# Performance work log

Measured on AMD Instinct MI355X. Metric: run time of the kernel, lower is better.

The kernel has to match this reference:

```python
import jax, jax.numpy as jnp
import numpy as np

WH, WW = 7, 7
DIM, HEADS = 256, 8


def make_table_index(wh, ww):
    # relative coords table (log-spaced CPB input) and relative position index
    ch = np.arange(-(wh - 1), wh, dtype=np.float32)
    cw = np.arange(-(ww - 1), ww, dtype=np.float32)
    t = np.stack(np.meshgrid(ch, cw, indexing='ij'), axis=-1)[None]  # [1,2wh-1,2ww-1,2]
    t = t.copy()
    t[..., 0] /= (wh - 1)
    t[..., 1] /= (ww - 1)
    t *= 8.0
    t = np.sign(t) * np.log2(np.abs(t) + 1.0) / np.log2(8.0)
    coords = np.stack(np.meshgrid(np.arange(wh), np.arange(ww), indexing='ij'))
    cf = coords.reshape(2, -1)
    rc = (cf[:, :, None] - cf[:, None, :]).transpose(1, 2, 0).copy()  # [N,N,2]
    rc[..., 0] += wh - 1
    rc[..., 1] += ww - 1
    rc[..., 0] *= 2 * ww - 1
    idx = rc.sum(-1)
    return t.astype(np.float32), idx.astype(np.int32)


def setup_inputs() -> dict:
    key = jax.random.key(0)
    ks = jax.random.split(key, 10)
    B_, N, C, H = 2048, WH * WW, DIM, HEADS
    table, idx = make_table_index(WH, WW)
    return {
        'x': jax.random.normal(ks[0], (B_, N, C), jnp.float32),
        'mask': jnp.zeros((64, N, N), jnp.float32),
        'qkv_w': jax.random.normal(ks[1], (3 * C, C), jnp.float32) * 0.02,
        'q_bias': jnp.zeros((C,), jnp.float32),
        'v_bias': jnp.zeros((C,), jnp.float32),
        'logit_scale': jnp.full((H, 1, 1), np.log(10.0), jnp.float32),
        'cpb_w1': jax.random.normal(ks[2], (512, 2), jnp.float32) * 0.02,
        'cpb_b1': jnp.zeros((512,), jnp.float32),
        'cpb_w2': jax.random.normal(ks[3], (H, 512), jnp.float32) * 0.02,
        'proj_w': jax.random.normal(ks[4], (C, C), jnp.float32) * 0.02,
        'proj_b': jnp.zeros((C,), jnp.float32),
        'rel_coords_table': jnp.asarray(table),
        'rel_pos_index': jnp.asarray(idx),
    }


def _l2norm(t):
    return t / jnp.maximum(jnp.linalg.norm(t, axis=-1, keepdims=True), 1e-12)


def reference(x, mask, qkv_w, q_bias, v_bias, logit_scale, cpb_w1, cpb_b1,
              cpb_w2, proj_w, proj_b, rel_coords_table, rel_pos_index):
    B_, N, C = x.shape
    H = logit_scale.shape[0]
    hd = C // H
    qkv_b = jnp.concatenate([q_bias, jnp.zeros_like(v_bias), v_bias])
    qkv = (x @ qkv_w.T + qkv_b).reshape(B_, N, 3, H, hd).transpose(2, 0, 3, 1, 4)
    q, k, v = qkv[0], qkv[1], qkv[2]  # [B_,H,N,hd]
    attn = jnp.einsum('bhnd,bhmd->bhnm', _l2norm(q), _l2norm(k))
    scale = jnp.exp(jnp.minimum(logit_scale, jnp.log(jnp.float32(100.0))))  # [H,1,1]
    attn = attn * scale[None]
    # CPB MLP -> relative position bias
    table = jax.nn.relu(rel_coords_table @ cpb_w1.T + cpb_b1) @ cpb_w2.T  # [1,Th,Tw,H]
    table = table.reshape(-1, H)
    bias = table[rel_pos_index.reshape(-1)].reshape(N, N, H).transpose(2, 0, 1)
    attn = attn + 16.0 * jax.nn.sigmoid(bias)[None]
    nW = mask.shape[0]
    attn = attn.reshape(B_ // nW, nW, H, N, N) + mask[None, :, None]
    attn = jax.nn.softmax(attn.reshape(B_, H, N, N), axis=-1)
    out = jnp.einsum('bhnm,bhmd->bhnd', attn, v).transpose(0, 2, 1, 3).reshape(B_, N, C)
    return out @ proj_w.T + proj_b
```

## Files before the change

### kernel.cpp

```cpp
#include <hip/hip_runtime.h>

#define DEV __device__ __forceinline__

typedef float  f32x4  __attribute__((ext_vector_type(4)));
typedef __bf16 bf16x4 __attribute__((ext_vector_type(4)));
typedef __bf16 bf16x8 __attribute__((ext_vector_type(8)));

DEV unsigned short f2bf(float f) {
  unsigned u = __float_as_uint(f);
  u += 0x7fffu + ((u >> 16) & 1u);
  return (unsigned short)(u >> 16);
}

DEV void cp16(const void* g, void* l) {
  __builtin_amdgcn_global_load_lds((const __attribute__((address_space(1))) void*)g,
                                   (__attribute__((address_space(3))) void*)l, 16, 0, 0);
}

__global__ __launch_bounds__(256) void prep_kernel(
    const float* __restrict__ qkv_w, const float* __restrict__ proj_w,
    const float* __restrict__ q_bias, const float* __restrict__ v_bias,
    unsigned short* __restrict__ wq, unsigned short* __restrict__ wp,
    float* __restrict__ qkvb)
{
  int gid = blockIdx.x * 256 + threadIdx.x;
  if (gid < 196608) wq[gid] = f2bf(qkv_w[gid]);
  else              wp[gid - 196608] = f2bf(proj_w[gid - 196608]);
  if (gid < 768)
    qkvb[gid] = (gid < 256) ? q_bias[gid] : ((gid < 512) ? 0.f : v_bias[gid - 512]);
}

__global__ __launch_bounds__(256) void xbf16(
    const float* __restrict__ X, unsigned short* __restrict__ Xb)
{
  size_t gid = (size_t)blockIdx.x * 256 + threadIdx.x;
  const float4* xp = (const float4*)X;
  float4 f0 = xp[2 * gid], f1 = xp[2 * gid + 1];
  bf16x8 u;
  u[0] = (__bf16)f0.x; u[1] = (__bf16)f0.y; u[2] = (__bf16)f0.z; u[3] = (__bf16)f0.w;
  u[4] = (__bf16)f1.x; u[5] = (__bf16)f1.y; u[6] = (__bf16)f1.z; u[7] = (__bf16)f1.w;
  ((bf16x8*)Xb)[gid] = u;
}

__global__ __launch_bounds__(64) void cpb_mlp(
    const float* __restrict__ tab, const float* __restrict__ w1,
    const float* __restrict__ b1, const float* __restrict__ w2,
    float* __restrict__ table16)
{
  int r = blockIdx.x;
  int t = threadIdx.x;
  float x0 = tab[r * 2 + 0], x1 = tab[r * 2 + 1];
  float part[8];
#pragma unroll
  for (int h = 0; h < 8; ++h) part[h] = 0.f;
  for (int j = t; j < 512; j += 64) {
    float hv = fmaxf(w1[j * 2 + 0] * x0 + w1[j * 2 + 1] * x1 + b1[j], 0.f);
#pragma unroll
    for (int h = 0; h < 8; ++h) part[h] += hv * w2[h * 512 + j];
  }
#pragma unroll
  for (int h = 0; h < 8; ++h) {
    float v = part[h];
    for (int off = 32; off > 0; off >>= 1) v += __shfl_down(v, off, 64);
    if (t == 0) table16[r * 8 + h] = 16.f / (1.f + expf(-v));
  }
}

__global__ __launch_bounds__(256) void bmb(
    const float* __restrict__ t16, const int* __restrict__ ridx,
    const float* __restrict__ mask, float* __restrict__ bias64,
    float* __restrict__ mask64)
{
  const float L2E = 1.44269504f;
  int gid = blockIdx.x * 256 + threadIdx.x;
  int p = gid & 4095, i = p >> 6, j = p & 63;
  bool valid = (i < 49) && (j < 49);
  if (gid < 32768) {
    int h = gid >> 12;
    bias64[gid] = valid ? t16[ridx[i * 49 + j] * 8 + h] * L2E : -1e30f;
  } else {
    int g2 = gid - 32768;
    int w = g2 >> 12;
    mask64[g2] = valid ? mask[w * 2401 + i * 49 + j] * L2E : 0.f;
  }
}

__global__ __launch_bounds__(256) void qkv_attn(
    const unsigned short* __restrict__ Xb, const unsigned short* __restrict__ W,
    const float* __restrict__ qkvb, const float* __restrict__ logit_scale,
    const float* __restrict__ bias64, const float* __restrict__ mask64,
    unsigned short* __restrict__ aout)
{
  __shared__ __align__(1024) char smem[65536];
  const int t = threadIdx.x, w = t >> 6, l = t & 63, quad = l >> 4, l15 = l & 15;
  char* sX  = smem;
  char* myr = smem + 32768 + w * 8192;

  const int win = blockIdx.x;
  const int wtok = win * 49;

  {
    const int r0 = w * 16;
    const int s = l & 31;
#pragma unroll
    for (int i = 0; i < 8; ++i) {
      const int row = r0 + 2 * i + (l >> 5);
      if (row < 49) {
        const unsigned short* src = Xb + (size_t)(wtok + row) * 256
                                  + (s >> 3) * 64 + (((s & 7) ^ (row & 7)) * 8);
        cp16(src, sX + (r0 + 2 * i) * 512);
      } else {
        uint4 z; z.x = z.y = z.z = z.w = 0u;
        *(uint4*)(sX + row * 512 + s * 16) = z;
      }
    }
  }
  __syncthreads();

  const int bslot = (quad ^ ((l15 >> 1) & 3)) * 16;

  auto do_gemm = [&](int wrb, f32x4 (&acc)[2][4]) {
#pragma unroll
    for (int kt = 0; kt < 4; ++kt)
#pragma unroll
      for (int kk = 0; kk < 2; ++kk) {
        bf16x8 wf[2], xf[4];
#pragma unroll
        for (int nt = 0; nt < 2; ++nt)
          wf[nt] = *(const bf16x8*)(W + (size_t)(wrb + nt * 16 + l15) * 256
                                      + kt * 64 + (4 * kk + quad) * 8);
#pragma unroll
        for (int mA = 0; mA < 4; ++mA)
          xf[mA] = *(const bf16x8*)(sX + (mA * 16 + l15) * 512 + kt * 128
                                       + (((4 * kk + quad) ^ (l15 & 7)) * 16));
#pragma unroll
        for (int nt = 0; nt < 2; ++nt)
#pragma unroll
          for (int mA = 0; mA < 4; ++mA)
            acc[nt][mA] = __builtin_amdgcn_mfma_f32_16x16x32_bf16(wf[nt], xf[mA], acc[nt][mA], 0, 0, 0);
      }
  };

  auto bounce = [&](f32x4 (&acc)[2][4], const float* bias, bf16x8 (&f)[4]) {
    const f32x4 b0 = *(const f32x4*)(bias + quad * 4);
    const f32x4 b1 = *(const f32x4*)(bias + 16 + quad * 4);
#pragma unroll
    for (int mA = 0; mA < 4; ++mA) {
      bf16x8 u;
      u[0] = (__bf16)(acc[0][mA][0] + b0[0]); u[1] = (__bf16)(acc[0][mA][1] + b0[1]);
      u[2] = (__bf16)(acc[0][mA][2] + b0[2]); u[3] = (__bf16)(acc[0][mA][3] + b0[3]);
      u[4] = (__bf16)(acc[1][mA][0] + b1[0]); u[5] = (__bf16)(acc[1][mA][1] + b1[1]);
      u[6] = (__bf16)(acc[1][mA][2] + b1[2]); u[7] = (__bf16)(acc[1][mA][3] + b1[3]);
      *(bf16x8*)(myr + (mA * 16 + l15) * 64 + bslot) = u;
    }
    asm volatile("s_waitcnt lgkmcnt(0)" ::: "memory");
    __builtin_amdgcn_sched_barrier(0);
#pragma unroll
    for (int mt = 0; mt < 4; ++mt)
      f[mt] = *(const bf16x8*)(myr + (mt * 16 + l15) * 64 + bslot);
  };

#pragma unroll 1
  for (int hh = 0; hh < 2; ++hh) {
    const int h = 2 * w + hh;

    f32x4 ka[2][4] = {};
    do_gemm(256 + h * 32, ka);
    bf16x8 kf[4];
    bounce(ka, qkvb + 256 + h * 32, kf);

    f32x4 qa[2][4] = {};
    do_gemm(h * 32, qa);
    bf16x8 qf[4];
    bounce(qa, qkvb + h * 32, qf);

    const float scale = __expf(fminf(logit_scale[h], 4.60517019f)) * 1.44269504f;
    float rqv[4];
#pragma unroll
    for (int nt = 0; nt < 4; ++nt) {
      float s = 0.f;
#pragma unroll
      for (int d = 0; d < 8; ++d) { float f = (float)qf[nt][d]; s += f * f; }
      s += __shfl_xor(s, 16, 64); s += __shfl_xor(s, 32, 64);
      rqv[nt] = scale / fmaxf(sqrtf(s), 1e-12f);
    }
    float rkl[4];
#pragma unroll
    for (int mt = 0; mt < 4; ++mt) {
      float s = 0.f;
#pragma unroll
      for (int d = 0; d < 8; ++d) { float f = (float)kf[mt][d]; s += f * f; }
      s += __shfl_xor(s, 16, 64); s += __shfl_xor(s, 32, 64);
      rkl[mt] = 1.f / fmaxf(sqrtf(s), 1e-12f);
    }
    f32x4 rk4v[4];
#pragma unroll
    for (int mt = 0; mt < 4; ++mt)
#pragma unroll
      for (int r = 0; r < 4; ++r)
        rk4v[mt][r] = __shfl(rkl[mt], (quad << 2) + r, 16);

    {
      f32x4 va[2][4] = {};
      do_gemm(512 + h * 32, va);
      const f32x4 vb0 = *(const f32x4*)(qkvb + 512 + h * 32 + quad * 4);
      const f32x4 vb1 = *(const f32x4*)(qkvb + 512 + h * 32 + 16 + quad * 4);
#pragma unroll
      for (int mA = 0; mA < 4; ++mA) {
        const int tok = mA * 16 + l15;
#pragma unroll
        for (int nt = 0; nt < 2; ++nt) {
#pragma unroll
          for (int r = 0; r < 4; ++r) {
            const int d = nt * 16 + quad * 4 + r;
            *(__bf16*)(myr + d * 128 + (((tok >> 3) ^ (d & 7)) << 4) + (tok & 7) * 2) =
                (__bf16)(va[nt][mA][r] + (nt ? vb1[r] : vb0[r]));
          }
        }
      }
    }
    asm volatile("s_waitcnt lgkmcnt(0)" ::: "memory");
    __builtin_amdgcn_sched_barrier(0);
    bf16x8 vf[2][2];
#pragma unroll
    for (int kk = 0; kk < 2; ++kk)
#pragma unroll
      for (int mt = 0; mt < 2; ++mt)
        vf[kk][mt] = *(const bf16x8*)(myr + (mt * 16 + l15) * 128
                                          + (((4 * kk + quad) ^ (l15 & 7)) * 16));
    asm volatile("s_waitcnt lgkmcnt(0)" ::: "memory");
    __builtin_amdgcn_sched_barrier(0);

    f32x4 sacc[4][4] = {};
    __builtin_amdgcn_s_setprio(1);
#pragma unroll
    for (int mt = 0; mt < 4; ++mt)
#pragma unroll
      for (int nt = 0; nt < 4; ++nt)
        sacc[mt][nt] = __builtin_amdgcn_mfma_f32_16x16x32_bf16(kf[mt], qf[nt], sacc[mt][nt], 0, 0, 0);
    __builtin_amdgcn_s_setprio(0);

    unsigned short* P = (unsigned short*)myr;
    const float* bh = bias64 + (size_t)h * 4096;
    const float* mw = mask64 + (size_t)(win & 63) * 4096;
    float rs4[4];
#pragma unroll
    for (int nt = 0; nt < 4; ++nt) {
      const int i = nt * 16 + l15;
      const float rqi = rqv[nt];
      float mx = -3e38f;
#pragma unroll
      for (int mt = 0; mt < 4; ++mt) {
        const int jb = mt * 16 + quad * 4;
        const f32x4 b4 = *(const f32x4*)(bh + i * 64 + jb);
        const f32x4 m4 = *(const f32x4*)(mw + i * 64 + jb);
#pragma unroll
        for (int r = 0; r < 4; ++r) {
          float sv = fmaf(sacc[mt][nt][r], rqi * rk4v[mt][r], b4[r] + m4[r]);
          sacc[mt][nt][r] = sv;
          mx = fmaxf(mx, sv);
        }
      }
      mx = fmaxf(mx, __shfl_xor(mx, 16, 64));
      mx = fmaxf(mx, __shfl_xor(mx, 32, 64));
      float sum = 0.f;
#pragma unroll
      for (int mt = 0; mt < 4; ++mt) {
        float pv[4];
#pragma unroll
        for (int r = 0; r < 4; ++r) {
          pv[r] = __builtin_amdgcn_exp2f(sacc[mt][nt][r] - mx);
          sum += pv[r];
        }
        bf16x4 pk;
        pk[0] = (__bf16)pv[0]; pk[1] = (__bf16)pv[1];
        pk[2] = (__bf16)pv[2]; pk[3] = (__bf16)pv[3];
        const int c = 2 * mt + (quad >> 1);
        *(bf16x4*)((char*)P + i * 128 + ((c ^ (i & 7)) * 16) + (quad & 1) * 8) = pk;
      }
      sum += __shfl_xor(sum, 16, 64);
      sum += __shfl_xor(sum, 32, 64);
      rs4[nt] = 1.f / sum;
    }
    asm volatile("s_waitcnt lgkmcnt(0)" ::: "memory");
    __builtin_amdgcn_sched_barrier(0);

    f32x4 oacc[2][4] = {};
#pragma unroll
    for (int kk = 0; kk < 2; ++kk) {
      bf16x8 pf[4];
#pragma unroll
      for (int nt = 0; nt < 4; ++nt)
        pf[nt] = *(const bf16x8*)((char*)P + (nt * 16 + l15) * 128
                                           + (((4 * kk + quad) ^ (l15 & 7)) * 16));
      __builtin_amdgcn_s_setprio(1);
#pragma unroll
      for (int mt = 0; mt < 2; ++mt)
#pragma unroll
        for (int nt = 0; nt < 4; ++nt)
          oacc[mt][nt] = __builtin_amdgcn_mfma_f32_16x16x32_bf16(vf[kk][mt], pf[nt], oacc[mt][nt], 0, 0, 0);
      __builtin_amdgcn_s_setprio(0);
    }

#pragma unroll
    for (int nt = 0; nt < 4; ++nt) {
      const int tok = nt * 16 + l15;
      if (tok < 49) {
        unsigned short* op = aout + (size_t)(wtok + tok) * 256 + h * 32;
        const float rs = rs4[nt];
#pragma unroll
        for (int mt = 0; mt < 2; ++mt) {
          bf16x4 ov;
          ov[0] = (__bf16)(oacc[mt][nt][0] * rs); ov[1] = (__bf16)(oacc[mt][nt][1] * rs);
          ov[2] = (__bf16)(oacc[mt][nt][2] * rs); ov[3] = (__bf16)(oacc[mt][nt][3] * rs);
          *(bf16x4*)(op + mt * 16 + quad * 4) = ov;
        }
      }
    }
  }
}

__global__ __launch_bounds__(256) void gemm_proj(
    const unsigned short* __restrict__ A, const unsigned short* __restrict__ W,
    const float* __restrict__ bias, float* __restrict__ Y)
{
  __shared__ __align__(1024) unsigned short sA[128 * 64];
  __shared__ __align__(1024) unsigned short sB[128 * 64];
  const int t = threadIdx.x, w = t >> 6, l = t & 63, quad = l >> 4, l15 = l & 15;
  const int bm = blockIdx.y * 128, bn = blockIdx.x * 128;
  const int wm = (w >> 1) * 64, wn = (w & 1) * 64;
  const int srow = t >> 3, sch = t & 7;
  const int sc = sch ^ (srow & 7);

  f32x4 acc[4][4] = {};
  for (int kt = 0; kt < 4; ++kt) {
    const int k0 = kt << 6;
    if (kt) __syncthreads();
#pragma unroll
    for (int i = 0; i < 4; ++i) {
      const int row = i * 32 + srow;
      cp16(A + (size_t)(bm + row) * 256 + k0 + sc * 8, sA + (i * 256 + w * 64) * 8);
      cp16(W + (size_t)(bn + row) * 256 + k0 + sc * 8, sB + (i * 256 + w * 64) * 8);
    }
    __syncthreads();
#pragma unroll
    for (int kk = 0; kk < 2; ++kk) {
      bf16x8 xf[4], wf[4];
#pragma unroll
      for (int mt = 0; mt < 4; ++mt)
        xf[mt] = *(const bf16x8*)&sA[(wm + mt * 16 + l15) * 64 + (((4 * kk + quad) ^ (l15 & 7)) * 8)];
#pragma unroll
      for (int nt = 0; nt < 4; ++nt)
        wf[nt] = *(const bf16x8*)&sB[(wn + nt * 16 + l15) * 64 + (((4 * kk + quad) ^ (l15 & 7)) * 8)];
#pragma unroll
      for (int nt = 0; nt < 4; ++nt)
#pragma unroll
        for (int mt = 0; mt < 4; ++mt)
          acc[nt][mt] = __builtin_amdgcn_mfma_f32_16x16x32_bf16(wf[nt], xf[mt], acc[nt][mt], 0, 0, 0);
    }
  }
#pragma unroll
  for (int mA = 0; mA < 4; ++mA) {
    const int row = bm + wm + mA * 16 + l15;
    float* orow = Y + (size_t)row * 256;
#pragma unroll
    for (int nW = 0; nW < 4; ++nW) {
      const int c0 = bn + wn + nW * 16 + quad * 4;
      const f32x4 bv = *(const f32x4*)(bias + c0);
      f32x4 v = acc[nW][mA];
      v[0] += bv[0]; v[1] += bv[1]; v[2] += bv[2]; v[3] += bv[3];
      *(f32x4*)(orow + c0) = v;
    }
  }
}

extern "C" void kernel_launch(void* const* d_in, const int* in_sizes, int n_in,
                              void* d_out, int out_size, void* d_ws, size_t ws_size,
                              hipStream_t stream) {
  const float* x           = (const float*)d_in[0];
  const float* mask        = (const float*)d_in[1];
  const float* qkv_w       = (const float*)d_in[2];
  const float* q_bias      = (const float*)d_in[3];
  const float* v_bias      = (const float*)d_in[4];
  const float* logit_scale = (const float*)d_in[5];
  const float* cpb_w1      = (const float*)d_in[6];
  const float* cpb_b1      = (const float*)d_in[7];
  const float* cpb_w2      = (const float*)d_in[8];
  const float* proj_w      = (const float*)d_in[9];
  const float* proj_b      = (const float*)d_in[10];
  const float* rel_tab     = (const float*)d_in[11];
  const int*   rel_idx     = (const int*)d_in[12];
  float*       out         = (float*)d_out;

  char* ws = (char*)d_ws;
  unsigned short* xbf     = (unsigned short*)(ws + 0);
  unsigned short* aows    = (unsigned short*)(ws + 154140672);
  unsigned short* wq      = (unsigned short*)(ws + 205520896);
  unsigned short* wp      = (unsigned short*)(ws + 205914112);
  float*          qkvb    = (float*)(ws + 206045184);
  float*          table16 = (float*)(ws + 206048256);
  float*          bias64  = (float*)(ws + 206053888);
  float*          mask64  = (float*)(ws + 206184960);

  prep_kernel<<<1024, 256, 0, stream>>>(qkv_w, proj_w, q_bias, v_bias, wq, wp, qkvb);
  cpb_mlp<<<169, 64, 0, stream>>>(rel_tab, cpb_w1, cpb_b1, cpb_w2, table16);
  bmb<<<1152, 256, 0, stream>>>(table16, rel_idx, mask, bias64, mask64);
  xbf16<<<12544, 256, 0, stream>>>(x, xbf);
  qkv_attn<<<2048, 256, 0, stream>>>(xbf, wq, qkvb, logit_scale, bias64, mask64, aows);
  gemm_proj<<<dim3(2, 784), 256, 0, stream>>>(aows, wp, proj_b, out);
}
```

Baseline: 413.3 us.

## Read X fragments directly from global, halve LDS, raise attention occupancy

The QKV-attention kernel stops staging the window's X tile in shared memory and loads the MFMA X fragments straight from global (L2-cached) bf16 data. This halves shared memory to 32KB and sets launch bounds to 4 blocks per CU, so more windows run concurrently. The xbf16 kernel now zero-pads a tail so the last window can read past 49 rows. K and Q are written to separate LDS slots before one wait, and the QK^T MFMAs are moved earlier to overlap with the V writes. The cost is uncoalesced, redundant global loads of X rows per wave, and the tighter occupancy target may force register spills.

```diff
diff --git a/kernel.cpp b/kernel.cpp
--- a/kernel.cpp
+++ b/kernel.cpp
@@ -34,12 +34,17 @@
     const float* __restrict__ X, unsigned short* __restrict__ Xb)
 {
   size_t gid = (size_t)blockIdx.x * 256 + threadIdx.x;
-  const float4* xp = (const float4*)X;
-  float4 f0 = xp[2 * gid], f1 = xp[2 * gid + 1];
-  bf16x8 u;
-  u[0] = (__bf16)f0.x; u[1] = (__bf16)f0.y; u[2] = (__bf16)f0.z; u[3] = (__bf16)f0.w;
-  u[4] = (__bf16)f1.x; u[5] = (__bf16)f1.y; u[6] = (__bf16)f1.z; u[7] = (__bf16)f1.w;
-  ((bf16x8*)Xb)[gid] = u;
+  if (gid < 3211264) {
+    const float4* xp = (const float4*)X;
+    float4 f0 = xp[2 * gid], f1 = xp[2 * gid + 1];
+    bf16x8 u;
+    u[0] = (__bf16)f0.x; u[1] = (__bf16)f0.y; u[2] = (__bf16)f0.z; u[3] = (__bf16)f0.w;
+    u[4] = (__bf16)f1.x; u[5] = (__bf16)f1.y; u[6] = (__bf16)f1.z; u[7] = (__bf16)f1.w;
+    ((bf16x8*)Xb)[gid] = u;
+  } else {
+    bf16x8 z = {};
+    ((bf16x8*)Xb)[gid] = z;
+  }
 }
 
 __global__ __launch_bounds__(64) void cpb_mlp(
@@ -85,38 +90,18 @@
   }
 }
 
-__global__ __launch_bounds__(256) void qkv_attn(
+__global__ __launch_bounds__(256, 4) void qkv_attn(
     const unsigned short* __restrict__ Xb, const unsigned short* __restrict__ W,
     const float* __restrict__ qkvb, const float* __restrict__ logit_scale,
     const float* __restrict__ bias64, const float* __restrict__ mask64,
     unsigned short* __restrict__ aout)
 {
-  __shared__ __align__(1024) char smem[65536];
+  __shared__ __align__(1024) char smem[32768];
   const int t = threadIdx.x, w = t >> 6, l = t & 63, quad = l >> 4, l15 = l & 15;
-  char* sX  = smem;
-  char* myr = smem + 32768 + w * 8192;
-
+  char* myr = smem + w * 8192;
   const int win = blockIdx.x;
   const int wtok = win * 49;
-
-  {
-    const int r0 = w * 16;
-    const int s = l & 31;
-#pragma unroll
-    for (int i = 0; i < 8; ++i) {
-      const int row = r0 + 2 * i + (l >> 5);
-      if (row < 49) {
-        const unsigned short* src = Xb + (size_t)(wtok + row) * 256
-                                  + (s >> 3) * 64 + (((s & 7) ^ (row & 7)) * 8);
-        cp16(src, sX + (r0 + 2 * i) * 512);
-      } else {
-        uint4 z; z.x = z.y = z.z = z.w = 0u;
-        *(uint4*)(sX + row * 512 + s * 16) = z;
-      }
-    }
-  }
-  __syncthreads();
-
+  const unsigned short* xrow = Xb + (size_t)wtok * 256;
   const int bslot = (quad ^ ((l15 >> 1) & 3)) * 16;
 
   auto do_gemm = [&](int wrb, f32x4 (&acc)[2][4]) {
@@ -124,15 +109,14 @@
     for (int kt = 0; kt < 4; ++kt)
 #pragma unroll
       for (int kk = 0; kk < 2; ++kk) {
+        const int co = kt * 64 + (4 * kk + quad) * 8;
         bf16x8 wf[2], xf[4];
 #pragma unroll
         for (int nt = 0; nt < 2; ++nt)
-          wf[nt] = *(const bf16x8*)(W + (size_t)(wrb + nt * 16 + l15) * 256
-                                      + kt * 64 + (4 * kk + quad) * 8);
+          wf[nt] = *(const bf16x8*)(W + (size_t)(wrb + nt * 16 + l15) * 256 + co);
 #pragma unroll
         for (int mA = 0; mA < 4; ++mA)
-          xf[mA] = *(const bf16x8*)(sX + (mA * 16 + l15) * 512 + kt * 128
-                                       + (((4 * kk + quad) ^ (l15 & 7)) * 16));
+          xf[mA] = *(const bf16x8*)(xrow + (size_t)(mA * 16 + l15) * 256 + co);
 #pragma unroll
         for (int nt = 0; nt < 2; ++nt)
 #pragma unroll
@@ -141,7 +125,7 @@
       }
   };
 
-  auto bounce = [&](f32x4 (&acc)[2][4], const float* bias, bf16x8 (&f)[4]) {
+  auto pack_write = [&](f32x4 (&acc)[2][4], const float* bias, char* dst) {
     const f32x4 b0 = *(const f32x4*)(bias + quad * 4);
     const f32x4 b1 = *(const f32x4*)(bias + 16 + quad * 4);
 #pragma unroll
@@ -151,13 +135,8 @@
       u[2] = (__bf16)(acc[0][mA][2] + b0[2]); u[3] = (__bf16)(acc[0][mA][3] + b0[3]);
       u[4] = (__bf16)(acc[1][mA][0] + b1[0]); u[5] = (__bf16)(acc[1][mA][1] + b1[1]);
       u[6] = (__bf16)(acc[1][mA][2] + b1[2]); u[7] = (__bf16)(acc[1][mA][3] + b1[3]);
-      *(bf16x8*)(myr + (mA * 16 + l15) * 64 + bslot) = u;
-    }
-    asm volatile("s_waitcnt lgkmcnt(0)" ::: "memory");
-    __builtin_amdgcn_sched_barrier(0);
-#pragma unroll
-    for (int mt = 0; mt < 4; ++mt)
-      f[mt] = *(const bf16x8*)(myr + (mt * 16 + l15) * 64 + bslot);
+      *(bf16x8*)(dst + (mA * 16 + l15) * 64 + bslot) = u;
+    }
   };
 
 #pragma unroll 1
@@ -166,13 +145,19 @@
 
     f32x4 ka[2][4] = {};
     do_gemm(256 + h * 32, ka);
-    bf16x8 kf[4];
-    bounce(ka, qkvb + 256 + h * 32, kf);
-
+    pack_write(ka, qkvb + 256 + h * 32, myr);
     f32x4 qa[2][4] = {};
     do_gemm(h * 32, qa);
-    bf16x8 qf[4];
-    bounce(qa, qkvb + h * 32, qf);
+    pack_write(qa, qkvb + h * 32, myr + 4096);
+    asm volatile("s_waitcnt lgkmcnt(0)" ::: "memory");
+    __builtin_amdgcn_sched_barrier(0);
+    bf16x8 kf[4], qf[4];
+#pragma unroll
+    for (int mt = 0; mt < 4; ++mt)
+      kf[mt] = *(const bf16x8*)(myr + (mt * 16 + l15) * 64 + bslot);
+#pragma unroll
+    for (int nt = 0; nt < 4; ++nt)
+      qf[nt] = *(const bf16x8*)(myr + 4096 + (nt * 16 + l15) * 64 + bslot);
 
     const float scale = __expf(fminf(logit_scale[h], 4.60517019f)) * 1.44269504f;
     float rqv[4];
@@ -219,6 +204,16 @@
         }
       }
     }
+
+    f32x4 sacc[4][4] = {};
+    __builtin_amdgcn_s_setprio(1);
+#pragma unroll
+    for (int mt = 0; mt < 4; ++mt)
+#pragma unroll
+      for (int nt = 0; nt < 4; ++nt)
+        sacc[mt][nt] = __builtin_amdgcn_mfma_f32_16x16x32_bf16(kf[mt], qf[nt], sacc[mt][nt], 0, 0, 0);
+    __builtin_amdgcn_s_setprio(0);
+
     asm volatile("s_waitcnt lgkmcnt(0)" ::: "memory");
     __builtin_amdgcn_sched_barrier(0);
     bf16x8 vf[2][2];
@@ -230,15 +225,6 @@
                                           + (((4 * kk + quad) ^ (l15 & 7)) * 16));
     asm volatile("s_waitcnt lgkmcnt(0)" ::: "memory");
     __builtin_amdgcn_sched_barrier(0);
-
-    f32x4 sacc[4][4] = {};
-    __builtin_amdgcn_s_setprio(1);
-#pragma unroll
-    for (int mt = 0; mt < 4; ++mt)
-#pragma unroll
-      for (int nt = 0; nt < 4; ++nt)
-        sacc[mt][nt] = __builtin_amdgcn_mfma_f32_16x16x32_bf16(kf[mt], qf[nt], sacc[mt][nt], 0, 0, 0);
-    __builtin_amdgcn_s_setprio(0);
 
     unsigned short* P = (unsigned short*)myr;
     const float* bh = bias64 + (size_t)h * 4096;
@@ -405,7 +391,7 @@
   prep_kernel<<<1024, 256, 0, stream>>>(qkv_w, proj_w, q_bias, v_bias, wq, wp, qkvb);
   cpb_mlp<<<169, 64, 0, stream>>>(rel_tab, cpb_w1, cpb_b1, cpb_w2, table16);
   bmb<<<1152, 256, 0, stream>>>(table16, rel_idx, mask, bias64, mask64);
-  xbf16<<<12544, 256, 0, stream>>>(x, xbf);
+  xbf16<<<12546, 256, 0, stream>>>(x, xbf);
   qkv_attn<<<2048, 256, 0, stream>>>(xbf, wq, qkvb, logit_scale, bias64, mask64, aows);
   gemm_proj<<<dim3(2, 784), 256, 0, stream>>>(aows, wp, proj_b, out);
 }
```

After: 843.6 us. 2.04x slower.
